# Performance work log

Hardware: AMD Instinct MI355X
Metric: run time of the kernel (lower is better)

Reference implementation:

```python
import jax, jax.numpy as jnp
import numpy as np

D_MODEL = 1024
H = 16
D_K = D_MODEL // H
D_FF = 4096
EPS = 1e-6


def setup_inputs() -> dict:
    key = jax.random.key(0)
    ks = jax.random.split(key, 16)
    s = 1.0 / np.sqrt(D_MODEL)
    sf = 1.0 / np.sqrt(D_FF)
    inp = {
        'x': jax.random.normal(ks[0], (4, 2048, D_MODEL), dtype=jnp.float32),
        'wq': jax.random.uniform(ks[1], (D_MODEL, D_MODEL), minval=-s, maxval=s),
        'bq': jax.random.uniform(ks[2], (D_MODEL,), minval=-s, maxval=s),
        'wk': jax.random.uniform(ks[3], (D_MODEL, D_MODEL), minval=-s, maxval=s),
        'bk': jax.random.uniform(ks[4], (D_MODEL,), minval=-s, maxval=s),
        'wv': jax.random.uniform(ks[5], (D_MODEL, D_MODEL), minval=-s, maxval=s),
        'bv': jax.random.uniform(ks[6], (D_MODEL,), minval=-s, maxval=s),
        'wo': jax.random.uniform(ks[7], (D_MODEL, D_MODEL), minval=-s, maxval=s),
        'bo': jax.random.uniform(ks[8], (D_MODEL,), minval=-s, maxval=s),
        'w1': jax.random.uniform(ks[9], (D_MODEL, D_FF), minval=-s, maxval=s),
        'b1': jax.random.uniform(ks[10], (D_FF,), minval=-s, maxval=s),
        'w2': jax.random.uniform(ks[11], (D_FF, D_MODEL), minval=-sf, maxval=sf),
        'b2': jax.random.uniform(ks[12], (D_MODEL,), minval=-sf, maxval=sf),
        'alpha1': jnp.ones((1,), jnp.float32),
        'bias1': jnp.zeros((1,), jnp.float32),
        'alpha2': jnp.ones((1,), jnp.float32),
        'bias2': jnp.zeros((1,), jnp.float32),
    }
    return inp


def _layer_norm(x, alpha, bias):
    # torch: alpha*(x-mean)/(std+eps)+bias with unbiased std (ddof=1), eps on std
    m = jnp.mean(x, axis=-1, keepdims=True)
    s = jnp.std(x, axis=-1, keepdims=True, ddof=1)
    return alpha * (x - m) / (s + EPS) + bias


def _mha(x, wq, bq, wk, bk, wv, bv, wo, bo):
    B, S, _ = x.shape
    q = (x @ wq + bq).reshape(B, S, H, D_K).transpose(0, 2, 1, 3)
    k = (x @ wk + bk).reshape(B, S, H, D_K).transpose(0, 2, 1, 3)
    v = (x @ wv + bv).reshape(B, S, H, D_K).transpose(0, 2, 1, 3)
    scores = jnp.einsum('bhqd,bhkd->bhqk', q, k) / np.sqrt(D_K)
    attn = jax.nn.softmax(scores, axis=-1)
    out = jnp.einsum('bhqk,bhkd->bhqd', attn, v)
    out = out.transpose(0, 2, 1, 3).reshape(B, S, D_MODEL)
    return out @ wo + bo


def reference(x, wq, bq, wk, bk, wv, bv, wo, bo, w1, b1, w2, b2,
              alpha1, bias1, alpha2, bias2):
    # Residual 1: x + MHA(LN(x))
    h = x + _mha(_layer_norm(x, alpha1, bias1), wq, bq, wk, bk, wv, bv, wo, bo)
    # Residual 2: h + FFN(LN(h)); FFN = W2 relu(W1 z + b1) + b2
    z = _layer_norm(h, alpha2, bias2)
    ffn = jax.nn.relu(z @ w1 + b1) @ w2 + b2
    return h + ffn
```

## Files before the change

kernel.cpp:

```cpp
#include <hip/hip_runtime.h>
#include <hip/hip_bf16.h>
#include <cstdint>
#include <cstddef>

typedef __bf16 bf16;
typedef __bf16 bf16x4 __attribute__((ext_vector_type(4)));
typedef __bf16 bf16x8 __attribute__((ext_vector_type(8)));
typedef float f32x4 __attribute__((ext_vector_type(4)));

#define QK_SCALE 0.1803368801111204f

#define AS1 __attribute__((address_space(1)))
#define AS3 __attribute__((address_space(3)))

__device__ __forceinline__ void gload_lds16(const void* g, void* l) {
  __builtin_amdgcn_global_load_lds((AS1 void*)g, (AS3 void*)l, 16, 0, 0);
}

__device__ __forceinline__ float b2f(unsigned short u) {
  union { unsigned int i; float f; } v; v.i = (unsigned int)u << 16; return v.f;
}

__global__ __launch_bounds__(256)
void transpose_cvt(const float* __restrict__ in, bf16* __restrict__ out,
                   int K, int N) {
  __shared__ float t[32][33];
  const int tx = threadIdx.x, ty = threadIdx.y;
  const int n0 = blockIdx.x * 32, k0 = blockIdx.y * 32;
#pragma unroll
  for (int j = ty; j < 32; j += 8)
    t[j][tx] = in[(size_t)(k0 + j) * N + n0 + tx];
  __syncthreads();
#pragma unroll
  for (int j = ty; j < 32; j += 8)
    out[(size_t)(n0 + j) * K + k0 + tx] = (bf16)t[tx][j];
}

__global__ __launch_bounds__(256)
void transpose_cvt4(const float* __restrict__ wq, const float* __restrict__ wk,
                    const float* __restrict__ wv, const float* __restrict__ wo,
                    bf16* __restrict__ wqkvT, bf16* __restrict__ woT) {
  __shared__ float t[32][33];
  const int tx = threadIdx.x, ty = threadIdx.y, z = blockIdx.z;
  const float* in = (z == 0) ? wq : (z == 1) ? wk : (z == 2) ? wv : wo;
  bf16* out = (z < 3) ? wqkvT + (size_t)z * 1024 * 1024 : woT;
  const float sc = (z == 0) ? QK_SCALE : 1.0f;
  const int n0 = blockIdx.x * 32, k0 = blockIdx.y * 32;
#pragma unroll
  for (int j = ty; j < 32; j += 8)
    t[j][tx] = in[(size_t)(k0 + j) * 1024 + n0 + tx] * sc;
  __syncthreads();
#pragma unroll
  for (int j = ty; j < 32; j += 8)
    out[(size_t)(n0 + j) * 1024 + k0 + tx] = (bf16)t[tx][j];
}

__global__ __launch_bounds__(256)
void concat_bias(const float* __restrict__ bq, const float* __restrict__ bk,
                 const float* __restrict__ bv, float* __restrict__ o) {
  int i = blockIdx.x * 256 + threadIdx.x;
  if (i < 1024) o[i] = bq[i] * QK_SCALE;
  else if (i < 2048) o[i] = bk[i - 1024];
  else o[i] = bv[i - 2048];
}

__global__ __launch_bounds__(256)
void ln_kernel(const float* __restrict__ x, bf16* __restrict__ y,
               const float* __restrict__ alpha_p, const float* __restrict__ beta_p) {
  const int row = blockIdx.x;
  const float4 v = ((const float4*)(x + (size_t)row * 1024))[threadIdx.x];
  float s = v.x + v.y + v.z + v.w;
  float ss = v.x * v.x + v.y * v.y + v.z * v.z + v.w * v.w;
#pragma unroll
  for (int m = 1; m < 64; m <<= 1) {
    s += __shfl_xor(s, m);
    ss += __shfl_xor(ss, m);
  }
  __shared__ float red[8];
  const int wave = threadIdx.x >> 6, lane = threadIdx.x & 63;
  if (lane == 0) { red[wave] = s; red[4 + wave] = ss; }
  __syncthreads();
  s = red[0] + red[1] + red[2] + red[3];
  ss = red[4] + red[5] + red[6] + red[7];
  const float mean = s * (1.0f / 1024.0f);
  const float var = fmaxf(ss - 1024.0f * mean * mean, 0.0f) * (1.0f / 1023.0f);
  const float k = alpha_p[0] / (sqrtf(var) + 1e-6f);
  const float beta = beta_p[0];
  union { bf16 b[4]; uint2 u; } pk;
  pk.b[0] = (bf16)((v.x - mean) * k + beta);
  pk.b[1] = (bf16)((v.y - mean) * k + beta);
  pk.b[2] = (bf16)((v.z - mean) * k + beta);
  pk.b[3] = (bf16)((v.w - mean) * k + beta);
  ((uint2*)(y + (size_t)row * 1024))[threadIdx.x] = pk.u;
}

template <typename OutT, bool RELU, bool RESID>
__global__ __launch_bounds__(256)
void gemm_bt(const bf16* __restrict__ A, const bf16* __restrict__ Bt,
             const float* __restrict__ bias, const float* __restrict__ resid,
             OutT* __restrict__ C, int M, int N, int K) {
  __shared__ __align__(16) bf16 As[2][128 * 32];
  __shared__ __align__(16) bf16 Bs[2][128 * 32];
  const int tid = threadIdx.x;
  const int wave = tid >> 6, lane = tid & 63;
  const int l16 = lane & 15, lq = lane >> 4;
  const int nwg = gridDim.x * gridDim.y;
  const int id = blockIdx.y * gridDim.x + blockIdx.x;
  const int w = (id & 7) * (nwg >> 3) + (id >> 3);
  const int bm = (w / gridDim.y) * 128, bn = (w % gridDim.y) * 128;
  const int wr = wave >> 1, wc = wave & 1;

  const int tmp = (lane * 16) ^ (((lane >> 3) & 7) << 4);
  const int srow = tmp >> 6, sseg = (tmp >> 4) & 3;
  const bf16* Ab = A + (size_t)bm * K + sseg * 8;
  const bf16* Bb = Bt + (size_t)bn * K + sseg * 8;

  auto STAGE = [&](int k0, int buf) {
#pragma unroll
    for (int i = 0; i < 2; i++) {
      const int chunk = wave * 2 + i;
      const int r = chunk * 16 + srow;
      gload_lds16(Ab + (size_t)r * K + k0, (char*)As[buf] + chunk * 1024);
      gload_lds16(Bb + (size_t)r * K + k0, (char*)Bs[buf] + chunk * 1024);
    }
  };
  auto swz = [&](int row) -> int {
    return (row >> 1) * 128 + (((((row & 1) << 2) | lq) ^ ((row >> 1) & 7)) << 4);
  };

  STAGE(0, 0);
  __syncthreads();

  f32x4 acc[4][4] = {};
  const int nk = K >> 5;
  for (int t = 0; t < nk; t++) {
    const int cur = t & 1;
    if (t + 1 < nk) STAGE((t + 1) << 5, cur ^ 1);
    bf16x8 a[4], b[4];
#pragma unroll
    for (int m = 0; m < 4; m++)
      a[m] = *(const bf16x8*)((const char*)As[cur] + swz(wr * 64 + m * 16 + l16));
#pragma unroll
    for (int n = 0; n < 4; n++)
      b[n] = *(const bf16x8*)((const char*)Bs[cur] + swz(wc * 64 + n * 16 + l16));
#pragma unroll
    for (int m = 0; m < 4; m++)
#pragma unroll
      for (int n = 0; n < 4; n++)
        acc[m][n] = __builtin_amdgcn_mfma_f32_16x16x32_bf16(a[m], b[n], acc[m][n], 0, 0, 0);
    __syncthreads();
  }
#pragma unroll
  for (int m = 0; m < 4; m++) {
    const int row0 = bm + wr * 64 + m * 16 + lq * 4;
#pragma unroll
    for (int n = 0; n < 4; n++) {
      const int col = bn + wc * 64 + n * 16 + l16;
      const float bv = bias[col];
#pragma unroll
      for (int j = 0; j < 4; j++) {
        float v = acc[m][n][j] + bv;
        if (RELU) v = fmaxf(v, 0.0f);
        if (RESID) v += resid[(size_t)(row0 + j) * N + col];
        C[(size_t)(row0 + j) * N + col] = (OutT)v;
      }
    }
  }
}

template <typename OutT, bool RELU, bool BIAS>
__global__ __launch_bounds__(512, 2)
void gemm_v4(const bf16* __restrict__ A, const bf16* __restrict__ Bt,
             const float* __restrict__ bias, OutT* __restrict__ C,
             int lda, int ldb, int ldc, int K,
             int azs, int bzs, size_t czs) {
  __shared__ __align__(16) char lds[3 * 32768];
  const int tid = threadIdx.x;
  const int wave = tid >> 6, lane = tid & 63;
  const int l16 = lane & 15, lq = lane >> 4;
  const int wr = wave >> 2, wc = wave & 3;
  const int nwg = gridDim.x * gridDim.y;
  const int id = blockIdx.y * gridDim.x + blockIdx.x;
  const int w = (id & 7) * (nwg >> 3) + (id >> 3);
  const int bm = (w / gridDim.y) * 256, bn = (w % gridDim.y) * 256;

  A  += (size_t)blockIdx.z * azs;
  Bt += (size_t)blockIdx.z * bzs;
  C  += (size_t)blockIdx.z * czs;

  const int p = lane >> 3, jj = (lane & 7) ^ p;
  const int lrow = p * 2 + (jj >> 2), lseg = jj & 3;
  const bf16* Abase = A + (size_t)bm * lda + lseg * 8;
  const bf16* Bbase = Bt + (size_t)bn * ldb + lseg * 8;

  auto STAGEQ = [&](int t, int qq) {
    const int k0 = t << 5;
    const int grow = (qq & 1) * 128 + wave * 16 + lrow;
    const void* src = (qq < 2) ? (const void*)(Abase + (size_t)grow * lda + k0)
                               : (const void*)(Bbase + (size_t)grow * ldb + k0);
    gload_lds16(src, lds + (t % 3) * 32768 + qq * 8192 + wave * 1024);
  };
  auto swz = [&](int row) -> int {
    return (row >> 1) * 128 + (((((row & 1) << 2) | lq) ^ ((row >> 1) & 7)) << 4);
  };

  const int nk = K >> 5;
#pragma unroll
  for (int qq = 0; qq < 4; qq++) STAGEQ(0, qq);
#pragma unroll
  for (int qq = 0; qq < 4; qq++) STAGEQ(1, qq);

  f32x4 acc[8][4] = {};
  for (int t = 0; t < nk; t++) {
    const char* buf = lds + (t % 3) * 32768;
    if (t + 1 < nk) asm volatile("s_waitcnt vmcnt(4)" ::: "memory");
    else            asm volatile("s_waitcnt vmcnt(0)" ::: "memory");
    __builtin_amdgcn_s_barrier();
    __builtin_amdgcn_sched_barrier(0);
    if (t + 2 < nk) { STAGEQ(t + 2, 0); STAGEQ(t + 2, 1); }
    bf16x8 a0[4], b0[4], a1[4];
#pragma unroll
    for (int i = 0; i < 4; i++)
      a0[i] = *(const bf16x8*)(buf + swz(wr * 128 + i * 16 + l16));
#pragma unroll
    for (int n = 0; n < 4; n++)
      b0[n] = *(const bf16x8*)(buf + 16384 + swz(wc * 64 + n * 16 + l16));
    if (t + 2 < nk) { STAGEQ(t + 2, 2); STAGEQ(t + 2, 3); }
#pragma unroll
    for (int i = 0; i < 4; i++)
      a1[i] = *(const bf16x8*)(buf + swz(wr * 128 + 64 + i * 16 + l16));
    __builtin_amdgcn_sched_barrier(0);
    __builtin_amdgcn_s_setprio(1);
#pragma unroll
    for (int i = 0; i < 4; i++)
#pragma unroll
      for (int n = 0; n < 4; n++)
        acc[i][n] = __builtin_amdgcn_mfma_f32_16x16x32_bf16(a0[i], b0[n], acc[i][n], 0, 0, 0);
    __builtin_amdgcn_s_setprio(0);
    __builtin_amdgcn_sched_barrier(0);
    __builtin_amdgcn_s_setprio(1);
#pragma unroll
    for (int i = 0; i < 4; i++)
#pragma unroll
      for (int n = 0; n < 4; n++)
        acc[4 + i][n] = __builtin_amdgcn_mfma_f32_16x16x32_bf16(a1[i], b0[n], acc[4 + i][n], 0, 0, 0);
    __builtin_amdgcn_s_setprio(0);
  }
#pragma unroll
  for (int m = 0; m < 8; m++) {
    const int row0 = bm + wr * 128 + m * 16 + lq * 4;
#pragma unroll
    for (int n = 0; n < 4; n++) {
      const int col = bn + wc * 64 + n * 16 + l16;
      const float bv = BIAS ? bias[col] : 0.0f;
#pragma unroll
      for (int j = 0; j < 4; j++) {
        float v = acc[m][n][j] + bv;
        if (RELU) v = fmaxf(v, 0.0f);
        C[(size_t)(row0 + j) * ldc + col] = (OutT)v;
      }
    }
  }
}

__global__ __launch_bounds__(256)
void ffn2_reduce(const bf16* __restrict__ p0, const bf16* __restrict__ p1,
                 const float* __restrict__ b2, float* __restrict__ out) {
  const size_t i = (size_t)blockIdx.x * 256 + threadIdx.x;
  float4 h = ((const float4*)out)[i];
  const ushort4 a = ((const ushort4*)p0)[i];
  const ushort4 b = ((const ushort4*)p1)[i];
  const float4 bb = ((const float4*)b2)[i & 255];
  h.x += b2f(a.x) + b2f(b.x) + bb.x;
  h.y += b2f(a.y) + b2f(b.y) + bb.y;
  h.z += b2f(a.z) + b2f(b.z) + bb.z;
  h.w += b2f(a.w) + b2f(b.w) + bb.w;
  ((float4*)out)[i] = h;
}

__global__ __launch_bounds__(256)
void vt_prep(const bf16* __restrict__ qkv, bf16* __restrict__ Vt) {
  __shared__ __align__(16) bf16 Vl[64 * 64];
  const int tid = threadIdx.x;
  const int sblk = blockIdx.x, bh = blockIdx.y, b = bh >> 4, h = bh & 15;
  const size_t srow = (size_t)b * 2048 + sblk * 64;
  const bf16* src = qkv + srow * 3072 + 2048 + h * 64;
#pragma unroll
  for (int i = 0; i < 2; i++) {
    int c = i * 256 + tid;
    int s = c >> 3, dseg = c & 7;
    int col = dseg ^ (s & 7) ^ (s >> 3);
    *(uint4*)((char*)Vl + s * 128 + col * 16) =
        *(const uint4*)(src + (size_t)s * 3072 + dseg * 8);
  }
  __syncthreads();
  bf16* dst = Vt + (size_t)bh * 64 * 2048 + sblk * 64;
#pragma unroll
  for (int i = 0; i < 2; i++) {
    int c = i * 256 + tid;
    int d = c >> 3, grp = c & 7;
    union { bf16 v[8]; uint4 u; } pk;
#pragma unroll
    for (int j = 0; j < 8; j++) {
      int pp = grp * 8 + j;
      int s = (pp & 32) | (((pp >> 2) & 1) << 4) | (((pp >> 3) & 3) << 2) | (pp & 3);
      int col = (d >> 3) ^ (s & 7) ^ (s >> 3);
      pk.v[j] = *(const bf16*)((char*)Vl + s * 128 + col * 16 + ((2 * d) & 15));
    }
    *(uint4*)(dst + (size_t)d * 2048 + grp * 8) = pk.u;
  }
}

__global__ __launch_bounds__(256, 2)
void attn_kernel(const bf16* __restrict__ qkv, const bf16* __restrict__ Vt,
                 bf16* __restrict__ out) {
  __shared__ __align__(16) bf16 smem[40960];
  bf16* Qs = smem;
  bf16* Ks = smem + 16384;
  bf16* Vs = smem + 28672;
  const int tid = threadIdx.x, wave = tid >> 6, lane = tid & 63;
  const int l16 = lane & 15, lq = lane >> 4;
  const int id = blockIdx.y * 8 + blockIdx.x;
  const int w = (id & 7) * 64 + (id >> 3);
  const int qblk = w & 7, bh = w >> 3;
  const int b = bh >> 4, h = bh & 15;
  const int q0 = qblk * 256;
  const size_t rowbase = (size_t)b * 2048;
  const bf16* Qg = qkv + (rowbase + q0) * 3072 + h * 64;
  const bf16* Kg = qkv + rowbase * 3072 + 1024 + h * 64;
  const bf16* Vg = Vt + (size_t)bh * 64 * 2048;

#pragma unroll
  for (int i = 0; i < 8; i++) {
    const int c = i * 256 + wave * 64;
    const int cl = c + lane;
    const int r = cl >> 3, seg = cl & 7;
    gload_lds16(Qg + (size_t)r * 3072 + (seg ^ (r & 7)) * 8, (char*)Qs + c * 16);
  }
  auto stageKV = [&](int kt, int buf) {
    const int kv0 = kt * 64;
#pragma unroll
    for (int i = 0; i < 2; i++) {
      const int c = i * 256 + wave * 64;
      const int cl = c + lane;
      const int r = cl >> 3, seg = cl & 7;
      gload_lds16(Kg + (size_t)(kv0 + r) * 3072 + (seg ^ (r & 7)) * 8,
                  (char*)Ks + buf * 8192 + c * 16);
      gload_lds16(Vg + (size_t)r * 2048 + kv0 + (seg ^ (r & 7)) * 8,
                  (char*)Vs + buf * 8192 + c * 16);
    }
  };
  stageKV(0, 0);
  stageKV(1, 1);

  asm volatile("s_waitcnt vmcnt(8)" ::: "memory");
  __builtin_amdgcn_s_barrier();
  bf16x8 qb[4][2];
#pragma unroll
  for (int g = 0; g < 4; g++)
#pragma unroll
    for (int H = 0; H < 2; H++) {
      const int row = wave * 64 + g * 16 + l16;
      const int col = (H * 64 + lq * 16) ^ ((row & 7) << 4);
      qb[g][H] = *(const bf16x8*)((const char*)Qs + row * 128 + col);
    }

  f32x4 oacc[4][4] = {};
  f32x4 lacc[4] = {};
  bf16x8 onesb;
#pragma unroll
  for (int j = 0; j < 8; j++) onesb[j] = (bf16)1.0f;

  for (int t = 0; t < 32; t++) {
    if (t < 31) asm volatile("s_waitcnt vmcnt(4)" ::: "memory");
    else        asm volatile("s_waitcnt vmcnt(0)" ::: "memory");
    __builtin_amdgcn_s_barrier();
    __builtin_amdgcn_sched_barrier(0);
    if (t + 2 < 32) stageKV(t + 2, (t + 2) % 3);
    const char* Kb = (const char*)Ks + (t % 3) * 8192;
    const char* Vb = (const char*)Vs + (t % 3) * 8192;

    bf16x8 ka[2][4];
#pragma unroll
    for (int H = 0; H < 2; H++)
#pragma unroll
      for (int m = 0; m < 4; m++) {
        const int row = m * 16 + l16;
        const int col = (H * 64 + lq * 16) ^ ((row & 7) << 4);
        ka[H][m] = *(const bf16x8*)(Kb + row * 128 + col);
      }
    bf16x8 vb[2][4];
#pragma unroll
    for (int H = 0; H < 2; H++)
#pragma unroll
      for (int nd = 0; nd < 4; nd++) {
        const int row = nd * 16 + l16;
        const int col = (H * 64 + lq * 16) ^ ((row & 7) << 4);
        vb[H][nd] = *(const bf16x8*)(Vb + row * 128 + col);
      }
#pragma unroll
    for (int g = 0; g < 4; g++) {
      f32x4 sc[4];
      __builtin_amdgcn_s_setprio(1);
#pragma unroll
      for (int m = 0; m < 4; m++) {
        f32x4 z = {};
        sc[m] = __builtin_amdgcn_mfma_f32_16x16x32_bf16(ka[0][m], qb[g][0], z, 0, 0, 0);
        sc[m] = __builtin_amdgcn_mfma_f32_16x16x32_bf16(ka[1][m], qb[g][1], sc[m], 0, 0, 0);
      }
      __builtin_amdgcn_s_setprio(0);
      bf16x8 pa0, pa1;
#pragma unroll
      for (int m = 0; m < 2; m++)
#pragma unroll
        for (int r = 0; r < 4; r++)
          pa0[m * 4 + r] = (bf16)__builtin_amdgcn_exp2f(sc[m][r]);
#pragma unroll
      for (int m = 0; m < 2; m++)
#pragma unroll
        for (int r = 0; r < 4; r++)
          pa1[m * 4 + r] = (bf16)__builtin_amdgcn_exp2f(sc[2 + m][r]);
      __builtin_amdgcn_s_setprio(1);
#pragma unroll
      for (int nd = 0; nd < 4; nd++) {
        oacc[g][nd] = __builtin_amdgcn_mfma_f32_16x16x32_bf16(pa0, vb[0][nd], oacc[g][nd], 0, 0, 0);
        oacc[g][nd] = __builtin_amdgcn_mfma_f32_16x16x32_bf16(pa1, vb[1][nd], oacc[g][nd], 0, 0, 0);
      }
      lacc[g] = __builtin_amdgcn_mfma_f32_16x16x32_bf16(pa0, onesb, lacc[g], 0, 0, 0);
      lacc[g] = __builtin_amdgcn_mfma_f32_16x16x32_bf16(pa1, onesb, lacc[g], 0, 0, 0);
      __builtin_amdgcn_s_setprio(0);
    }
  }
#pragma unroll
  for (int g = 0; g < 4; g++) {
#pragma unroll
    for (int r = 0; r < 4; r++) {
      const float inv = 1.0f / lacc[g][r];
      const size_t row = rowbase + q0 + wave * 64 + g * 16 + lq * 4 + r;
#pragma unroll
      for (int nd = 0; nd < 4; nd++)
        out[row * 1024 + h * 64 + nd * 16 + l16] = (bf16)(oacc[g][nd][r] * inv);
    }
  }
}

extern "C" void kernel_launch(void* const* d_in, const int* in_sizes, int n_in,
                              void* d_out, int out_size, void* d_ws, size_t ws_size,
                              hipStream_t stream) {
  const float* x      = (const float*)d_in[0];
  const float* wq     = (const float*)d_in[1];
  const float* bq     = (const float*)d_in[2];
  const float* wk     = (const float*)d_in[3];
  const float* bk     = (const float*)d_in[4];
  const float* wv     = (const float*)d_in[5];
  const float* bv     = (const float*)d_in[6];
  const float* wo     = (const float*)d_in[7];
  const float* bo     = (const float*)d_in[8];
  const float* w1     = (const float*)d_in[9];
  const float* b1     = (const float*)d_in[10];
  const float* w2     = (const float*)d_in[11];
  const float* b2     = (const float*)d_in[12];
  const float* alpha1 = (const float*)d_in[13];
  const float* bias1  = (const float*)d_in[14];
  const float* alpha2 = (const float*)d_in[15];
  const float* bias2  = (const float*)d_in[16];
  float* out = (float*)d_out;

  const size_t MB = 1024ull * 1024ull;
  char* ws = (char*)d_ws;
  bf16*  wqkvT = (bf16*)(ws);
  bf16*  woT   = (bf16*)(ws + 6 * MB);
  bf16*  w1T   = (bf16*)(ws + 8 * MB);
  bf16*  w2T   = (bf16*)(ws + 16 * MB);
  float* bqkv  = (float*)(ws + 24 * MB);
  bf16*  Z     = (bf16*)(ws + 24 * MB + 65536);
  bf16*  Vtb   = Z;
  bf16*  QKV   = (bf16*)(ws + 40 * MB + 65536);
  bf16*  AO    = (bf16*)(ws + 88 * MB + 65536);
  bf16*  FFN1  = QKV;
  bf16*  PART  = (bf16*)ws;
  const size_t PART1_OFF = (24 * MB + 65536) / 2;

  const dim3 tb(32, 8);
  transpose_cvt4<<<dim3(32, 32, 4), tb, 0, stream>>>(wq, wk, wv, wo, wqkvT, woT);
  transpose_cvt<<<dim3(128, 32), tb, 0, stream>>>(w1, w1T, 1024, 4096);
  transpose_cvt<<<dim3(32, 128), tb, 0, stream>>>(w2, w2T, 4096, 1024);
  concat_bias<<<12, 256, 0, stream>>>(bq, bk, bv, bqkv);

  ln_kernel<<<8192, 256, 0, stream>>>(x, Z, alpha1, bias1);
  gemm_v4<bf16, false, true><<<dim3(32, 12), 512, 0, stream>>>(
      Z, wqkvT, bqkv, QKV, 1024, 1024, 3072, 1024, 0, 0, 0);
  vt_prep<<<dim3(32, 64), 256, 0, stream>>>(QKV, Vtb);
  attn_kernel<<<dim3(8, 64), 256, 0, stream>>>(QKV, Vtb, AO);
  gemm_bt<float, false, true><<<dim3(64, 8), 256, 0, stream>>>(
      AO, woT, bo, x, out, 8192, 1024, 1024);
  ln_kernel<<<8192, 256, 0, stream>>>(out, Z, alpha2, bias2);
  gemm_v4<bf16, true, true><<<dim3(32, 16), 512, 0, stream>>>(
      Z, w1T, b1, FFN1, 1024, 1024, 4096, 1024, 0, 0, 0);
  gemm_v4<bf16, false, false><<<dim3(32, 4, 2), 512, 0, stream>>>(
      FFN1, w2T, nullptr, PART, 4096, 4096, 1024, 2048, 2048, 2048, PART1_OFF);
  ffn2_reduce<<<8192, 256, 0, stream>>>(PART, PART + PART1_OFF, b2, out);
}
```

Before: 352.0 us.

## Replace GEMM kernels with unified 128x256-tile double-buffered kernel

```diff
diff --git a/kernel.cpp b/kernel.cpp
--- a/kernel.cpp
+++ b/kernel.cpp
@@ -94,87 +94,13 @@
   ((uint2*)(y + (size_t)row * 1024))[threadIdx.x] = pk.u;
 }
 
-template <typename OutT, bool RELU, bool RESID>
-__global__ __launch_bounds__(256)
-void gemm_bt(const bf16* __restrict__ A, const bf16* __restrict__ Bt,
+template <typename OutT, bool RELU, bool BIAS, bool RESID>
+__global__ __launch_bounds__(512, 4)
+void gemm_v5(const bf16* __restrict__ A, const bf16* __restrict__ Bt,
              const float* __restrict__ bias, const float* __restrict__ resid,
-             OutT* __restrict__ C, int M, int N, int K) {
-  __shared__ __align__(16) bf16 As[2][128 * 32];
-  __shared__ __align__(16) bf16 Bs[2][128 * 32];
-  const int tid = threadIdx.x;
-  const int wave = tid >> 6, lane = tid & 63;
-  const int l16 = lane & 15, lq = lane >> 4;
-  const int nwg = gridDim.x * gridDim.y;
-  const int id = blockIdx.y * gridDim.x + blockIdx.x;
-  const int w = (id & 7) * (nwg >> 3) + (id >> 3);
-  const int bm = (w / gridDim.y) * 128, bn = (w % gridDim.y) * 128;
-  const int wr = wave >> 1, wc = wave & 1;
-
-  const int tmp = (lane * 16) ^ (((lane >> 3) & 7) << 4);
-  const int srow = tmp >> 6, sseg = (tmp >> 4) & 3;
-  const bf16* Ab = A + (size_t)bm * K + sseg * 8;
-  const bf16* Bb = Bt + (size_t)bn * K + sseg * 8;
-
-  auto STAGE = [&](int k0, int buf) {
-#pragma unroll
-    for (int i = 0; i < 2; i++) {
-      const int chunk = wave * 2 + i;
-      const int r = chunk * 16 + srow;
-      gload_lds16(Ab + (size_t)r * K + k0, (char*)As[buf] + chunk * 1024);
-      gload_lds16(Bb + (size_t)r * K + k0, (char*)Bs[buf] + chunk * 1024);
-    }
-  };
-  auto swz = [&](int row) -> int {
-    return (row >> 1) * 128 + (((((row & 1) << 2) | lq) ^ ((row >> 1) & 7)) << 4);
-  };
-
-  STAGE(0, 0);
-  __syncthreads();
-
-  f32x4 acc[4][4] = {};
-  const int nk = K >> 5;
-  for (int t = 0; t < nk; t++) {
-    const int cur = t & 1;
-    if (t + 1 < nk) STAGE((t + 1) << 5, cur ^ 1);
-    bf16x8 a[4], b[4];
-#pragma unroll
-    for (int m = 0; m < 4; m++)
-      a[m] = *(const bf16x8*)((const char*)As[cur] + swz(wr * 64 + m * 16 + l16));
-#pragma unroll
-    for (int n = 0; n < 4; n++)
-      b[n] = *(const bf16x8*)((const char*)Bs[cur] + swz(wc * 64 + n * 16 + l16));
-#pragma unroll
-    for (int m = 0; m < 4; m++)
-#pragma unroll
-      for (int n = 0; n < 4; n++)
-        acc[m][n] = __builtin_amdgcn_mfma_f32_16x16x32_bf16(a[m], b[n], acc[m][n], 0, 0, 0);
-    __syncthreads();
-  }
-#pragma unroll
-  for (int m = 0; m < 4; m++) {
-    const int row0 = bm + wr * 64 + m * 16 + lq * 4;
-#pragma unroll
-    for (int n = 0; n < 4; n++) {
-      const int col = bn + wc * 64 + n * 16 + l16;
-      const float bv = bias[col];
-#pragma unroll
-      for (int j = 0; j < 4; j++) {
-        float v = acc[m][n][j] + bv;
-        if (RELU) v = fmaxf(v, 0.0f);
-        if (RESID) v += resid[(size_t)(row0 + j) * N + col];
-        C[(size_t)(row0 + j) * N + col] = (OutT)v;
-      }
-    }
-  }
-}
-
-template <typename OutT, bool RELU, bool BIAS>
-__global__ __launch_bounds__(512, 2)
-void gemm_v4(const bf16* __restrict__ A, const bf16* __restrict__ Bt,
-             const float* __restrict__ bias, OutT* __restrict__ C,
-             int lda, int ldb, int ldc, int K,
+             OutT* __restrict__ C, int lda, int ldb, int ldc, int K,
              int azs, int bzs, size_t czs) {
-  __shared__ __align__(16) char lds[3 * 32768];
+  __shared__ __align__(16) char lds[2][24576];
   const int tid = threadIdx.x;
   const int wave = tid >> 6, lane = tid & 63;
   const int l16 = lane & 15, lq = lane >> 4;
@@ -182,7 +108,7 @@
   const int nwg = gridDim.x * gridDim.y;
   const int id = blockIdx.y * gridDim.x + blockIdx.x;
   const int w = (id & 7) * (nwg >> 3) + (id >> 3);
-  const int bm = (w / gridDim.y) * 256, bn = (w % gridDim.y) * 256;
+  const int bm = (w / gridDim.y) * 128, bn = (w % gridDim.y) * 256;
 
   A  += (size_t)blockIdx.z * azs;
   Bt += (size_t)blockIdx.z * bzs;
@@ -193,62 +119,46 @@
   const bf16* Abase = A + (size_t)bm * lda + lseg * 8;
   const bf16* Bbase = Bt + (size_t)bn * ldb + lseg * 8;
 
-  auto STAGEQ = [&](int t, int qq) {
+  auto STAGE = [&](int t, int slot) {
     const int k0 = t << 5;
-    const int grow = (qq & 1) * 128 + wave * 16 + lrow;
-    const void* src = (qq < 2) ? (const void*)(Abase + (size_t)grow * lda + k0)
-                               : (const void*)(Bbase + (size_t)grow * ldb + k0);
-    gload_lds16(src, lds + (t % 3) * 32768 + qq * 8192 + wave * 1024);
+    gload_lds16(Abase + (size_t)(wave * 16 + lrow) * lda + k0,
+                lds[slot] + wave * 1024);
+#pragma unroll
+    for (int i = 0; i < 2; i++) {
+      const int ch = wave * 2 + i;
+      gload_lds16(Bbase + (size_t)(ch * 16 + lrow) * ldb + k0,
+                  lds[slot] + 8192 + ch * 1024);
+    }
   };
   auto swz = [&](int row) -> int {
     return (row >> 1) * 128 + (((((row & 1) << 2) | lq) ^ ((row >> 1) & 7)) << 4);
   };
 
-  const int nk = K >> 5;
-#pragma unroll
-  for (int qq = 0; qq < 4; qq++) STAGEQ(0, qq);
-#pragma unroll
-  for (int qq = 0; qq < 4; qq++) STAGEQ(1, qq);
-
-  f32x4 acc[8][4] = {};
-  for (int t = 0; t < nk; t++) {
-    const char* buf = lds + (t % 3) * 32768;
-    if (t + 1 < nk) asm volatile("s_waitcnt vmcnt(4)" ::: "memory");
-    else            asm volatile("s_waitcnt vmcnt(0)" ::: "memory");
-    __builtin_amdgcn_s_barrier();
-    __builtin_amdgcn_sched_barrier(0);
-    if (t + 2 < nk) { STAGEQ(t + 2, 0); STAGEQ(t + 2, 1); }
-    bf16x8 a0[4], b0[4], a1[4];
-#pragma unroll
-    for (int i = 0; i < 4; i++)
-      a0[i] = *(const bf16x8*)(buf + swz(wr * 128 + i * 16 + l16));
-#pragma unroll
-    for (int n = 0; n < 4; n++)
-      b0[n] = *(const bf16x8*)(buf + 16384 + swz(wc * 64 + n * 16 + l16));
-    if (t + 2 < nk) { STAGEQ(t + 2, 2); STAGEQ(t + 2, 3); }
-#pragma unroll
-    for (int i = 0; i < 4; i++)
-      a1[i] = *(const bf16x8*)(buf + swz(wr * 128 + 64 + i * 16 + l16));
-    __builtin_amdgcn_sched_barrier(0);
-    __builtin_amdgcn_s_setprio(1);
-#pragma unroll
-    for (int i = 0; i < 4; i++)
-#pragma unroll
-      for (int n = 0; n < 4; n++)
-        acc[i][n] = __builtin_amdgcn_mfma_f32_16x16x32_bf16(a0[i], b0[n], acc[i][n], 0, 0, 0);
-    __builtin_amdgcn_s_setprio(0);
-    __builtin_amdgcn_sched_barrier(0);
-    __builtin_amdgcn_s_setprio(1);
-#pragma unroll
-    for (int i = 0; i < 4; i++)
-#pragma unroll
-      for (int n = 0; n < 4; n++)
-        acc[4 + i][n] = __builtin_amdgcn_mfma_f32_16x16x32_bf16(a1[i], b0[n], acc[4 + i][n], 0, 0, 0);
-    __builtin_amdgcn_s_setprio(0);
-  }
-#pragma unroll
-  for (int m = 0; m < 8; m++) {
-    const int row0 = bm + wr * 128 + m * 16 + lq * 4;
+  const int nkt = K >> 5;
+  STAGE(0, 0);
+  __syncthreads();
+
+  f32x4 acc[4][4] = {};
+  for (int t = 0; t < nkt; t++) {
+    const int cur = t & 1;
+    if (t + 1 < nkt) STAGE(t + 1, cur ^ 1);
+    bf16x8 a[4];
+#pragma unroll
+    for (int m = 0; m < 4; m++)
+      a[m] = *(const bf16x8*)(lds[cur] + swz(wr * 64 + m * 16 + l16));
+#pragma unroll
+    for (int n = 0; n < 4; n++) {
+      const bf16x8 b =
+          *(const bf16x8*)(lds[cur] + 8192 + swz(wc * 64 + n * 16 + l16));
+#pragma unroll
+      for (int m = 0; m < 4; m++)
+        acc[m][n] = __builtin_amdgcn_mfma_f32_16x16x32_bf16(a[m], b, acc[m][n], 0, 0, 0);
+    }
+    __syncthreads();
+  }
+#pragma unroll
+  for (int m = 0; m < 4; m++) {
+    const int row0 = bm + wr * 64 + m * 16 + lq * 4;
 #pragma unroll
     for (int n = 0; n < 4; n++) {
       const int col = bn + wc * 64 + n * 16 + l16;
@@ -257,6 +167,7 @@
       for (int j = 0; j < 4; j++) {
         float v = acc[m][n][j] + bv;
         if (RELU) v = fmaxf(v, 0.0f);
+        if (RESID) v += resid[(size_t)(row0 + j) * ldc + col];
         C[(size_t)(row0 + j) * ldc + col] = (OutT)v;
       }
     }
@@ -488,16 +399,16 @@
   concat_bias<<<12, 256, 0, stream>>>(bq, bk, bv, bqkv);
 
   ln_kernel<<<8192, 256, 0, stream>>>(x, Z, alpha1, bias1);
-  gemm_v4<bf16, false, true><<<dim3(32, 12), 512, 0, stream>>>(
-      Z, wqkvT, bqkv, QKV, 1024, 1024, 3072, 1024, 0, 0, 0);
+  gemm_v5<bf16, false, true, false><<<dim3(64, 12), 512, 0, stream>>>(
+      Z, wqkvT, bqkv, nullptr, QKV, 1024, 1024, 3072, 1024, 0, 0, 0);
   vt_prep<<<dim3(32, 64), 256, 0, stream>>>(QKV, Vtb);
   attn_kernel<<<dim3(8, 64), 256, 0, stream>>>(QKV, Vtb, AO);
-  gemm_bt<float, false, true><<<dim3(64, 8), 256, 0, stream>>>(
-      AO, woT, bo, x, out, 8192, 1024, 1024);
+  gemm_v5<float, false, true, true><<<dim3(64, 4), 512, 0, stream>>>(
+      AO, woT, bo, x, out, 1024, 1024, 1024, 1024, 0, 0, 0);
   ln_kernel<<<8192, 256, 0, stream>>>(out, Z, alpha2, bias2);
-  gemm_v4<bf16, true, true><<<dim3(32, 16), 512, 0, stream>>>(
-      Z, w1T, b1, FFN1, 1024, 1024, 4096, 1024, 0, 0, 0);
-  gemm_v4<bf16, false, false><<<dim3(32, 4, 2), 512, 0, stream>>>(
-      FFN1, w2T, nullptr, PART, 4096, 4096, 1024, 2048, 2048, 2048, PART1_OFF);
+  gemm_v5<bf16, true, true, false><<<dim3(64, 16), 512, 0, stream>>>(
+      Z, w1T, b1, nullptr, FFN1, 1024, 1024, 4096, 1024, 0, 0, 0);
+  gemm_v5<bf16, false, false, false><<<dim3(64, 4, 2), 512, 0, stream>>>(
+      FFN1, w2T, nullptr, nullptr, PART, 4096, 4096, 1024, 2048, 2048, 2048, PART1_OFF);
   ffn2_reduce<<<8192, 256, 0, stream>>>(PART, PART + PART1_OFF, b2, out);
 }
```

New measurement: 359.6 us. 1.02x slower.
